# Optimization experiments

Hardware: AMD Instinct MI355X
Metric: run time of the kernel (lower is better)

Reference implementation:

```python
import jax, jax.numpy as jnp
import numpy as np

N_HEADS = 8
NEG_INF = -1e30  # finite stand-in for -inf in masked_fill (exact 0 prob after softmax)


def apply_rotary_emb(x, cos, sin):
    # x: [B, H, T, hd]; cos/sin: [T, hd] -> broadcast over B, H
    d = x.shape[-1]
    x1, x2 = x[..., : d // 2], x[..., d // 2 :]
    x_rot = jnp.concatenate((-x2, x1), axis=-1)
    return x * cos[None, None] + x_rot * sin[None, None]


def setup_inputs() -> dict:
    key = jax.random.key(0)
    ks = jax.random.split(key, 5)
    B, T, C, hd = 4, 2048, 512, 64
    x = jax.random.normal(ks[0], (B, T, C), dtype=jnp.float32)
    cos = jax.random.uniform(ks[1], (T, hd), dtype=jnp.float32)
    sin = jax.random.uniform(ks[2], (T, hd), dtype=jnp.float32)
    # xavier_uniform-ish scale for linear weights
    W_qkv = jax.random.normal(ks[3], (3 * C, C), dtype=jnp.float32) * (1.0 / np.sqrt(C))
    W_out = jax.random.normal(ks[4], (C, C), dtype=jnp.float32) * (1.0 / np.sqrt(C))
    return {"x": x, "cos": cos, "sin": sin, "W_qkv": W_qkv, "W_out": W_out}


def reference(x, cos, sin, W_qkv, W_out):
    B, T, C = x.shape
    H = N_HEADS
    hd = C // H
    # qkv projection (torch Linear: y = x @ W^T), split into q, k, v as [B, H, T, hd]
    qkv = (x @ W_qkv.T).reshape(B, T, 3, H, hd)
    qkv = jnp.transpose(qkv, (2, 0, 3, 1, 4))
    q, k, v = qkv[0], qkv[1], qkv[2]
    # RoPE on q, k
    q = apply_rotary_emb(q, cos[:T], sin[:T])
    k = apply_rotary_emb(k, cos[:T], sin[:T])
    scale = jnp.sqrt(jnp.float32(hd))
    attn = jnp.einsum("bhqd,bhkd->bhqk", q, k) / scale  # [B, H, T, T]
    causal = jnp.tril(jnp.ones((T, T), dtype=bool))
    attn = jnp.where(causal[None, None], attn, NEG_INF)
    attn = jax.nn.softmax(attn, axis=-1)
    out = jnp.einsum("bhqk,bhkd->bhqd", attn, v)  # [B, H, T, hd]
    out = jnp.transpose(out, (0, 2, 1, 3)).reshape(B, T, C)
    return out @ W_out.T
```

## Files before the change

kernel.cpp:

```cpp
#include <hip/hip_runtime.h>
#include <hip/hip_bf16.h>

#define B_SZ 4
#define T_SZ 2048
#define C_SZ 512
#define H_SZ 8
#define HD 64
#define QSCALE 0.1803368801111137f

typedef __bf16 bf16;
typedef __bf16 bf16x8 __attribute__((ext_vector_type(8)));
typedef float f32x4 __attribute__((ext_vector_type(4)));

__device__ __forceinline__ f32x4 mfma16(bf16x8 a, bf16x8 b, f32x4 c) {
    return __builtin_amdgcn_mfma_f32_16x16x32_bf16(a, b, c, 0, 0, 0);
}

#define GLD_LDS16(g, l) __builtin_amdgcn_global_load_lds( \
    (__attribute__((address_space(1))) void*)(void*)(g),  \
    (__attribute__((address_space(3))) void*)(l), 16, 0, 0)

__global__ __launch_bounds__(256) void cvt_all(
    const float* __restrict__ x, const float* __restrict__ wqkv,
    const float* __restrict__ wout, bf16* __restrict__ xb,
    bf16* __restrict__ wqb, bf16* __restrict__ wob) {
  int i = blockIdx.x * 256 + threadIdx.x;
  const int n0 = (B_SZ*T_SZ*C_SZ)/4, n1 = (3*C_SZ*C_SZ)/4, n2 = (C_SZ*C_SZ)/4;
  const float4* s; bf16* d; int j;
  if (i < n0)                { s = (const float4*)x;    d = xb;  j = i; }
  else if (i < n0 + n1)      { s = (const float4*)wqkv; d = wqb; j = i - n0; }
  else if (i < n0 + n1 + n2) { s = (const float4*)wout; d = wob; j = i - n0 - n1; }
  else return;
  float4 v = s[j];
  union { bf16 h[4]; uint2 u; } p;
  p.h[0] = (bf16)v.x; p.h[1] = (bf16)v.y; p.h[2] = (bf16)v.z; p.h[3] = (bf16)v.w;
  *(uint2*)(d + (size_t)j * 4) = p.u;
}

template<int EPI>
__global__ __launch_bounds__(256) void gemm_bt(
    const bf16* __restrict__ A, const bf16* __restrict__ Bw,
    int M, int N, int K,
    void* __restrict__ o0, void* __restrict__ o1, void* __restrict__ o2) {
  __shared__ bf16 sA[128 * 32];
  __shared__ bf16 sB[128 * 32];
  const int tid = threadIdx.x;
  const int m0 = blockIdx.x * 128, n0 = blockIdx.y * 128;
  const int w = tid >> 6, lane = tid & 63, quad = lane >> 4, l16 = lane & 15;
  const int wm = (w >> 1) * 64, wn = (w & 1) * 64;
  const int srow = tid >> 2, scol = (tid & 3) * 8;
  f32x4 acc[4][4] = {};
  for (int k0 = 0; k0 < K; k0 += 32) {
    __syncthreads();
    const bf16* ga = A  + (size_t)(m0 + srow) * K + k0 + scol;
    const bf16* gb = Bw + (size_t)(n0 + srow) * K + k0 + scol;
    GLD_LDS16(ga,                 sA + tid * 8);
    GLD_LDS16(ga + (size_t)64*K,  sA + tid * 8 + 2048);
    GLD_LDS16(gb,                 sB + tid * 8);
    GLD_LDS16(gb + (size_t)64*K,  sB + tid * 8 + 2048);
    __syncthreads();
    bf16x8 af[4], bfr[4];
#pragma unroll
    for (int i = 0; i < 4; i++)
      af[i] = *(const bf16x8*)(sA + (wm + i*16 + l16) * 32 + quad * 8);
#pragma unroll
    for (int j = 0; j < 4; j++)
      bfr[j] = *(const bf16x8*)(sB + (wn + j*16 + l16) * 32 + quad * 8);
#pragma unroll
    for (int i = 0; i < 4; i++)
#pragma unroll
      for (int j = 0; j < 4; j++)
        acc[i][j] = mfma16(af[i], bfr[j], acc[i][j]);
  }
  if (EPI == 0) {
    const int three = n0 >> 9;
    bf16* dst = three == 0 ? (bf16*)o0 : (three == 1 ? (bf16*)o1 : (bf16*)o2);
#pragma unroll
    for (int i = 0; i < 4; i++) {
#pragma unroll
      for (int j = 0; j < 4; j++) {
        const int n = n0 + wn + j*16 + l16;
        const int h = (n & 511) >> 6, dcol = n & 63;
#pragma unroll
        for (int r = 0; r < 4; r++) {
          const int m = m0 + wm + i*16 + quad*4 + r;
          const int b = m >> 11, t = m & (T_SZ - 1);
          if (three < 2)
            dst[(((size_t)(b*H_SZ + h)) * T_SZ + t) * HD + dcol] = (bf16)acc[i][j][r];
          else
            dst[(((size_t)(b*H_SZ + h)) * HD + dcol) * T_SZ + t] = (bf16)acc[i][j][r];
        }
      }
    }
  } else {
    float* dst = (float*)o0;
#pragma unroll
    for (int i = 0; i < 4; i++)
#pragma unroll
      for (int j = 0; j < 4; j++)
#pragma unroll
        for (int r = 0; r < 4; r++) {
          const int m = m0 + wm + i*16 + quad*4 + r;
          const int n = n0 + wn + j*16 + l16;
          dst[(size_t)m * N + n] = acc[i][j][r];
        }
  }
}

__global__ __launch_bounds__(256) void rope_qk(
    bf16* __restrict__ q, bf16* __restrict__ k,
    const float* __restrict__ cp, const float* __restrict__ sp) {
  const int i = blockIdx.x * 256 + threadIdx.x;
  const int d  = i & 31;
  const int t  = (i >> 5) & (T_SZ - 1);
  const int bh = i >> 16;
  const size_t base = ((size_t)bh * T_SZ + t) * HD;
  const float c1 = cp[t*HD + d], c2 = cp[t*HD + d + 32];
  const float s1 = sp[t*HD + d], s2 = sp[t*HD + d + 32];
  float a = (float)q[base + d], b = (float)q[base + d + 32];
  q[base + d]      = (bf16)((a * c1 - b * s1) * QSCALE);
  q[base + d + 32] = (bf16)((b * c2 + a * s2) * QSCALE);
  a = (float)k[base + d]; b = (float)k[base + d + 32];
  k[base + d]      = (bf16)(a * c1 - b * s1);
  k[base + d + 32] = (bf16)(b * c2 + a * s2);
}

__global__ __launch_bounds__(256) void flash_attn(
    const bf16* __restrict__ qb, const bf16* __restrict__ kb,
    const bf16* __restrict__ vtb, bf16* __restrict__ ao) {
  __shared__ bf16 sK[2][64 * 64];
  __shared__ bf16 sVT[2][64 * 64];
  __shared__ bf16 sP[4][2560];
  const int tid = threadIdx.x, w = tid >> 6, lane = tid & 63;
  const int quad = lane >> 4, l16 = lane & 15;
  const int bh = blockIdx.x & 31;
  const int pj = blockIdx.x >> 5;
  const int nA = (16 - pj) * 2;
  const int ntot = 34;
  int qi = 15 - pj;
  int q0w = qi * 128 + w * 32;
  const bf16* Q  = qb  + (size_t)bh * T_SZ * HD;
  const bf16* Kp = kb  + (size_t)bh * T_SZ * HD;
  const bf16* Vt = vtb + (size_t)bh * HD * T_SZ;
  bf16x8 qf[2][2];
#pragma unroll
  for (int nt = 0; nt < 2; nt++)
#pragma unroll
    for (int ds = 0; ds < 2; ds++)
      qf[nt][ds] = *(const bf16x8*)(Q + (size_t)(q0w + nt*16 + l16) * HD + ds*32 + quad*8);
  float l_[2] = {0.f, 0.f};
  f32x4 ot[4][2] = {};
  bf16* sPw = &sP[w][0];
  const int srow = tid >> 3, scg = (tid & 7) ^ (srow & 7);
  const int b = bh >> 3, h = bh & 7;

  auto epilogue = [&]() {
    float lt[2];
#pragma unroll
    for (int nt = 0; nt < 2; nt++) {
      float s = l_[nt];
      s += __shfl_xor(s, 16);
      s += __shfl_xor(s, 32);
      lt[nt] = 1.f / s;
    }
#pragma unroll
    for (int dt = 0; dt < 4; dt++)
#pragma unroll
      for (int nt = 0; nt < 2; nt++) {
        union { bf16 h4[4]; unsigned long long ull; } pk;
#pragma unroll
        for (int r = 0; r < 4; r++) pk.h4[r] = (bf16)(ot[dt][nt][r] * lt[nt]);
        *(unsigned long long*)(sPw + (nt*16 + l16)*72 + dt*16 + quad*4) = pk.ull;
      }
    asm volatile("" ::: "memory");
    const int oq = lane >> 1, half = lane & 1;
    const int tg = qi*128 + w*32 + oq;
    bf16* dst = ao + ((size_t)(b * T_SZ + tg)) * C_SZ + h * HD + half * 32;
#pragma unroll
    for (int j = 0; j < 4; j++)
      *(uint4*)(dst + j*8) = *(const uint4*)(sPw + oq*72 + half*32 + j*8);
    asm volatile("" ::: "memory");
  };

  GLD_LDS16(Kp + (size_t)srow * HD + scg*8,          sK[0]  + tid*8);
  GLD_LDS16(Kp + (size_t)(srow + 32) * HD + scg*8,   sK[0]  + tid*8 + 2048);
  GLD_LDS16(Vt + (size_t)srow * T_SZ + scg*8,        sVT[0] + tid*8);
  GLD_LDS16(Vt + (size_t)(srow + 32) * T_SZ + scg*8, sVT[0] + tid*8 + 2048);

  for (int it = 0; it < ntot; it++) {
    const int kt = (it < nA ? it : it - nA) * 64;
    __syncthreads();
    if (it + 1 < ntot) {
      const int kn = (it + 1 < nA ? it + 1 : it + 1 - nA) * 64;
      bf16* dK = sK[(it + 1) & 1];
      bf16* dV = sVT[(it + 1) & 1];
      GLD_LDS16(Kp + (size_t)(kn + srow) * HD + scg*8,        dK + tid*8);
      GLD_LDS16(Kp + (size_t)(kn + srow + 32) * HD + scg*8,   dK + tid*8 + 2048);
      GLD_LDS16(Vt + (size_t)srow * T_SZ + kn + scg*8,        dV + tid*8);
      GLD_LDS16(Vt + (size_t)(srow + 32) * T_SZ + kn + scg*8, dV + tid*8 + 2048);
    }
    if (kt <= q0w + 31) {
      const bf16* cK = sK[it & 1];
      const bf16* cV = sVT[it & 1];
      f32x4 st[4][2] = {};
#pragma unroll
      for (int mt = 0; mt < 4; mt++) {
#pragma unroll
        for (int ds = 0; ds < 2; ds++) {
          const int row = mt*16 + l16, cl = ds*4 + quad;
          const bf16x8 kf = *(const bf16x8*)(cK + row*64 + (cl ^ (row & 7)) * 8);
#pragma unroll
          for (int nt = 0; nt < 2; nt++)
            st[mt][nt] = mfma16(kf, qf[nt][ds], st[mt][nt]);
        }
      }
      if (kt + 63 > q0w) {
#pragma unroll
        for (int nt = 0; nt < 2; nt++) {
          const int qg = q0w + nt*16 + l16;
          const int kb0 = kt + quad*4;
#pragma unroll
          for (int mt = 0; mt < 4; mt++)
#pragma unroll
            for (int r = 0; r < 4; r++)
              st[mt][nt][r] = (kb0 + mt*16 + r <= qg) ? st[mt][nt][r] : -1e30f;
        }
      }
#pragma unroll
      for (int nt = 0; nt < 2; nt++) {
        float sum = 0.f;
#pragma unroll
        for (int mt = 0; mt < 4; mt++) {
          union { bf16 h4[4]; unsigned long long ull; } pk;
#pragma unroll
          for (int r = 0; r < 4; r++) {
            const float p = __builtin_amdgcn_exp2f(st[mt][nt][r]);
            sum += p;
            pk.h4[r] = (bf16)p;
          }
          *(unsigned long long*)(sPw + (mt>>1)*1280 + (nt*16 + l16)*40 + (mt&1)*16 + quad*4) = pk.ull;
        }
        l_[nt] += sum;
      }
      asm volatile("" ::: "memory");
      bf16x8 pf[2][2];
#pragma unroll
      for (int nt = 0; nt < 2; nt++)
#pragma unroll
        for (int s = 0; s < 2; s++)
          pf[nt][s] = *(const bf16x8*)(sPw + s*1280 + (nt*16 + l16)*40 + quad*8);
#pragma unroll
      for (int dt = 0; dt < 4; dt++) {
#pragma unroll
        for (int s = 0; s < 2; s++) {
          const int row = dt*16 + l16, cl = s*4 + quad;
          const bf16x8 vf = *(const bf16x8*)(cV + row*64 + (cl ^ (row & 7)) * 8);
#pragma unroll
          for (int nt = 0; nt < 2; nt++)
            ot[dt][nt] = mfma16(vf, pf[nt][s], ot[dt][nt]);
        }
      }
    }
    if (it == nA - 1) {
      epilogue();
      qi = pj; q0w = qi * 128 + w * 32;
#pragma unroll
      for (int nt = 0; nt < 2; nt++)
#pragma unroll
        for (int ds = 0; ds < 2; ds++)
          qf[nt][ds] = *(const bf16x8*)(Q + (size_t)(q0w + nt*16 + l16) * HD + ds*32 + quad*8);
      l_[0] = 0.f; l_[1] = 0.f;
#pragma unroll
      for (int dt = 0; dt < 4; dt++)
#pragma unroll
        for (int nt = 0; nt < 2; nt++)
          ot[dt][nt] = f32x4{0.f, 0.f, 0.f, 0.f};
    }
  }
  epilogue();
}

extern "C" void kernel_launch(void* const* d_in, const int* in_sizes, int n_in,
                              void* d_out, int out_size, void* d_ws, size_t ws_size,
                              hipStream_t stream) {
  const float* x    = (const float*)d_in[0];
  const float* cosp = (const float*)d_in[1];
  const float* sinp = (const float*)d_in[2];
  const float* wqkv = (const float*)d_in[3];
  const float* wout = (const float*)d_in[4];
  char* ws = (char*)d_ws;
  bf16* xb    = (bf16*)(ws);
  bf16* wqkvb = (bf16*)(ws +  8388608);
  bf16* woutb = (bf16*)(ws +  9961472);
  bf16* qbuf  = (bf16*)(ws + 10485760);
  bf16* kbuf  = (bf16*)(ws + 18874368);
  bf16* vtbuf = (bf16*)(ws + 27262976);
  bf16* ao    = (bf16*)(ws + 35651584);

  cvt_all<<<dim3(5120), dim3(256), 0, stream>>>(x, wqkv, wout, xb, wqkvb, woutb);
  gemm_bt<0><<<dim3(64, 12), dim3(256), 0, stream>>>(
      xb, wqkvb, B_SZ * T_SZ, 3 * C_SZ, C_SZ,
      (void*)qbuf, (void*)kbuf, (void*)vtbuf);
  rope_qk<<<dim3(8192), dim3(256), 0, stream>>>(qbuf, kbuf, cosp, sinp);
  flash_attn<<<dim3(256), dim3(256), 0, stream>>>(qbuf, kbuf, vtbuf, ao);
  gemm_bt<1><<<dim3(64, 4), dim3(256), 0, stream>>>(
      ao, woutb, B_SZ * T_SZ, C_SZ, C_SZ,
      (void*)d_out, nullptr, nullptr);
}
```

Before: 177.0 us.

## Split flash attention work per block in two halves with combine kernel

Each attention workgroup's 34 key-tile iterations are split across two workgroups, giving 512 blocks instead of 256 so more of the GPU's compute units stay busy. The half covering the long query tile writes unnormalized partial outputs and row sums to a workspace, and a new combine kernel adds the two partials and normalizes. No max-subtraction is used, so summing the partials stays consistent. The cost is an extra launch, extra global traffic for the partials, and a bf16 rounding of the partial outputs. The old x bf16 buffer is reused as scratch.

```diff
diff --git a/kernel.cpp b/kernel.cpp
--- a/kernel.cpp
+++ b/kernel.cpp
@@ -127,16 +127,19 @@
 
 __global__ __launch_bounds__(256) void flash_attn(
     const bf16* __restrict__ qb, const bf16* __restrict__ kb,
-    const bf16* __restrict__ vtb, bf16* __restrict__ ao) {
+    const bf16* __restrict__ vtb, bf16* __restrict__ ao,
+    bf16* __restrict__ Oa, float* __restrict__ lbuf) {
   __shared__ bf16 sK[2][64 * 64];
   __shared__ bf16 sVT[2][64 * 64];
   __shared__ bf16 sP[4][2560];
   const int tid = threadIdx.x, w = tid >> 6, lane = tid & 63;
   const int quad = lane >> 4, l16 = lane & 15;
   const int bh = blockIdx.x & 31;
-  const int pj = blockIdx.x >> 5;
+  const int ph = blockIdx.x >> 5;
+  const int pj = ph >> 1;
+  const int halfb = ph & 1;
   const int nA = (16 - pj) * 2;
-  const int ntot = 34;
+  const int i0 = halfb * 17, i1 = i0 + 17;
   int qi = 15 - pj;
   int q0w = qi * 128 + w * 32;
   const bf16* Q  = qb  + (size_t)bh * T_SZ * HD;
@@ -153,8 +156,34 @@
   bf16* sPw = &sP[w][0];
   const int srow = tid >> 3, scg = (tid & 7) ^ (srow & 7);
   const int b = bh >> 3, h = bh & 7;
-
-  auto epilogue = [&]() {
+  const int recA = (pj * 32 + bh) * 2;
+
+  auto partial_epilogue = [&](int slot) {
+#pragma unroll
+    for (int nt = 0; nt < 2; nt++) {
+      float s = l_[nt];
+      s += __shfl_xor(s, 16);
+      s += __shfl_xor(s, 32);
+      if (quad == 0) lbuf[(recA + slot) * 128 + w*32 + nt*16 + l16] = s;
+    }
+#pragma unroll
+    for (int dt = 0; dt < 4; dt++)
+#pragma unroll
+      for (int nt = 0; nt < 2; nt++) {
+        union { bf16 h4[4]; unsigned long long ull; } pk;
+#pragma unroll
+        for (int r = 0; r < 4; r++) pk.h4[r] = (bf16)ot[dt][nt][r];
+        *(unsigned long long*)(sPw + (nt*16 + l16)*72 + dt*16 + quad*4) = pk.ull;
+      }
+    asm volatile("" ::: "memory");
+    const int oq = lane >> 1, hf = lane & 1;
+    bf16* dst = Oa + (size_t)(recA + slot) * 8192 + (w*32 + oq) * 64 + hf * 32;
+#pragma unroll
+    for (int j = 0; j < 4; j++)
+      *(uint4*)(dst + j*8) = *(const uint4*)(sPw + oq*72 + hf*32 + j*8);
+    asm volatile("" ::: "memory");
+  };
+  auto final_epilogue = [&]() {
     float lt[2];
 #pragma unroll
     for (int nt = 0; nt < 2; nt++) {
@@ -173,24 +202,28 @@
         *(unsigned long long*)(sPw + (nt*16 + l16)*72 + dt*16 + quad*4) = pk.ull;
       }
     asm volatile("" ::: "memory");
-    const int oq = lane >> 1, half = lane & 1;
+    const int oq = lane >> 1, hf = lane & 1;
     const int tg = qi*128 + w*32 + oq;
-    bf16* dst = ao + ((size_t)(b * T_SZ + tg)) * C_SZ + h * HD + half * 32;
+    bf16* dst = ao + ((size_t)(b * T_SZ + tg)) * C_SZ + h * HD + hf * 32;
 #pragma unroll
     for (int j = 0; j < 4; j++)
-      *(uint4*)(dst + j*8) = *(const uint4*)(sPw + oq*72 + half*32 + j*8);
-    asm volatile("" ::: "memory");
+      *(uint4*)(dst + j*8) = *(const uint4*)(sPw + oq*72 + hf*32 + j*8);
   };
 
-  GLD_LDS16(Kp + (size_t)srow * HD + scg*8,          sK[0]  + tid*8);
-  GLD_LDS16(Kp + (size_t)(srow + 32) * HD + scg*8,   sK[0]  + tid*8 + 2048);
-  GLD_LDS16(Vt + (size_t)srow * T_SZ + scg*8,        sVT[0] + tid*8);
-  GLD_LDS16(Vt + (size_t)(srow + 32) * T_SZ + scg*8, sVT[0] + tid*8 + 2048);
-
-  for (int it = 0; it < ntot; it++) {
+  {
+    const int kt0 = i0 * 64;
+    bf16* dK = sK[i0 & 1];
+    bf16* dV = sVT[i0 & 1];
+    GLD_LDS16(Kp + (size_t)(kt0 + srow) * HD + scg*8,        dK + tid*8);
+    GLD_LDS16(Kp + (size_t)(kt0 + srow + 32) * HD + scg*8,   dK + tid*8 + 2048);
+    GLD_LDS16(Vt + (size_t)srow * T_SZ + kt0 + scg*8,        dV + tid*8);
+    GLD_LDS16(Vt + (size_t)(srow + 32) * T_SZ + kt0 + scg*8, dV + tid*8 + 2048);
+  }
+
+  for (int it = i0; it < i1; it++) {
     const int kt = (it < nA ? it : it - nA) * 64;
     __syncthreads();
-    if (it + 1 < ntot) {
+    if (it + 1 < i1) {
       const int kn = (it + 1 < nA ? it + 1 : it + 1 - nA) * 64;
       bf16* dK = sK[(it + 1) & 1];
       bf16* dV = sVT[(it + 1) & 1];
@@ -262,7 +295,7 @@
       }
     }
     if (it == nA - 1) {
-      epilogue();
+      partial_epilogue(1);
       qi = pj; q0w = qi * 128 + w * 32;
 #pragma unroll
       for (int nt = 0; nt < 2; nt++)
@@ -277,7 +310,33 @@
           ot[dt][nt] = f32x4{0.f, 0.f, 0.f, 0.f};
     }
   }
-  epilogue();
+  if (halfb == 0) partial_epilogue(0);
+  else            final_epilogue();
+}
+
+__global__ __launch_bounds__(256) void combine_o(
+    const bf16* __restrict__ Oa, const float* __restrict__ lbuf,
+    bf16* __restrict__ ao) {
+  const int inst = blockIdx.x;
+  const int bh = inst & 31, pj = inst >> 5;
+  const int b = bh >> 3, h = bh & 7;
+  const int t = threadIdx.x;
+  const int q = t >> 1, d0 = (t & 1) * 32;
+  const bf16* p0 = Oa + ((size_t)inst*2    ) * 8192 + q*64 + d0;
+  const bf16* p1 = Oa + ((size_t)inst*2 + 1) * 8192 + q*64 + d0;
+  const float inv = 1.f / (lbuf[(inst*2)*128 + q] + lbuf[(inst*2+1)*128 + q]);
+  const int tg = (15 - pj) * 128 + q;
+  bf16* dst = ao + ((size_t)(b*T_SZ + tg)) * C_SZ + h*HD + d0;
+#pragma unroll
+  for (int c = 0; c < 4; c++) {
+    union { uint4 u; bf16 h8[8]; } a, bb, o;
+    a.u  = *(const uint4*)(p0 + c*8);
+    bb.u = *(const uint4*)(p1 + c*8);
+#pragma unroll
+    for (int j = 0; j < 8; j++)
+      o.h8[j] = (bf16)(((float)a.h8[j] + (float)bb.h8[j]) * inv);
+    *(uint4*)(dst + c*8) = o.u;
+  }
 }
 
 extern "C" void kernel_launch(void* const* d_in, const int* in_sizes, int n_in,
@@ -296,13 +355,16 @@
   bf16* kbuf  = (bf16*)(ws + 18874368);
   bf16* vtbuf = (bf16*)(ws + 27262976);
   bf16* ao    = (bf16*)(ws + 35651584);
+  bf16* Oa    = xb;
+  float* lbuf = (float*)(ws + 44040192);
 
   cvt_all<<<dim3(5120), dim3(256), 0, stream>>>(x, wqkv, wout, xb, wqkvb, woutb);
   gemm_bt<0><<<dim3(64, 12), dim3(256), 0, stream>>>(
       xb, wqkvb, B_SZ * T_SZ, 3 * C_SZ, C_SZ,
       (void*)qbuf, (void*)kbuf, (void*)vtbuf);
   rope_qk<<<dim3(8192), dim3(256), 0, stream>>>(qbuf, kbuf, cosp, sinp);
-  flash_attn<<<dim3(256), dim3(256), 0, stream>>>(qbuf, kbuf, vtbuf, ao);
+  flash_attn<<<dim3(512), dim3(256), 0, stream>>>(qbuf, kbuf, vtbuf, ao, Oa, lbuf);
+  combine_o<<<dim3(256), dim3(256), 0, stream>>>(Oa, lbuf, ao);
   gemm_bt<1><<<dim3(64, 4), dim3(256), 0, stream>>>(
       ao, woutb, B_SZ * T_SZ, C_SZ, C_SZ,
       (void*)d_out, nullptr, nullptr);
```

Measured after the change: 163.9 us. 1.08x faster.
